# Kernel optimization log

Measured on AMD Instinct MI355X. Metric: run time of the kernel, lower is better.

Reference implementation:

```python
import jax, jax.numpy as jnp
import numpy as np
from jax import lax

B, T = 64, 2048
D_LSTM, D_ENC, D_ATT, N_F, K = 1024, 512, 128, 32, 31
PAD = (K - 1) // 2  # 15, 'same' padding as Tacotron2 LocationLayer


def setup_inputs() -> dict:
    key = jax.random.key(0)
    ks = jax.random.split(key, 11)
    def w(k, shape, fan_in):
        return jax.random.normal(k, shape, dtype=jnp.float32) / np.sqrt(fan_in)
    return {
        "query": jax.random.normal(ks[0], (B, 1, D_LSTM), dtype=jnp.float32),
        "memory": jax.random.normal(ks[1], (B, T, D_ENC), dtype=jnp.float32),
        "attention_weights_cat": jax.random.uniform(ks[2], (B, 2, T), dtype=jnp.float32),
        "Wq": w(ks[3], (D_ATT, D_LSTM), D_LSTM),
        "bq": jnp.zeros((D_ATT,), jnp.float32),
        "Wm": w(ks[4], (D_ATT, D_ENC), D_ENC),
        "bm": jnp.zeros((D_ATT,), jnp.float32),
        "Wconv": w(ks[5], (N_F, 2, K), 2 * K),  # Conv1d weight [out, in, k], bias=False
        "Wloc": w(ks[6], (D_ATT, N_F), N_F),     # location dense, bias=False
        "Wv": w(ks[7], (1, D_ATT), D_ATT),
        "bv": jnp.zeros((1,), jnp.float32),
    }


def reference(query, memory, attention_weights_cat, Wq, bq, Wm, bm, Wconv, Wloc, Wv, bv):
    # query_layer: [B,1,D_LSTM] -> [B,1,D_ATT]
    q = query @ Wq.T + bq
    # memory_layer: [B,T,D_ENC] -> [B,T,D_ATT]
    k = memory @ Wm.T + bm
    # location_layer: Conv1d same-pad over time, then dense to D_ATT
    conv = lax.conv_general_dilated(
        attention_weights_cat, Wconv, window_strides=(1,),
        padding=[(PAD, PAD)], dimension_numbers=("NCH", "OIH", "NCH"))  # [B,N_F,T]
    loc = jnp.einsum("bft,af->bta", conv, Wloc)  # [B,T,D_ATT]
    # energies: v^T tanh(q + k + loc) -> [B,T]
    energies = (jnp.tanh(q + k + loc) @ Wv.T + bv).squeeze(-1)
    attention_weights = jax.nn.softmax(energies, axis=1)  # [B,T]
    attention_context = jnp.einsum("bt,btd->bd", attention_weights, memory)  # [B,D_ENC]
    return attention_context, attention_weights
```

## Files before the change

kernel.cpp:

```cpp
#include <hip/hip_runtime.h>
#include <math.h>

#define B_ 64
#define T_ 2048
#define DL 1024
#define DE 512
#define DA 128
#define NF 32
#define KW 31
#define PADW 15
#define TT 128

typedef short bf16x8 __attribute__((ext_vector_type(8)));
typedef float f32x4 __attribute__((ext_vector_type(4)));

__device__ __forceinline__ void split_bf16(float x, unsigned short &hi, unsigned short &lo) {
    unsigned u = __float_as_uint(x);
    unsigned short h = (unsigned short)((u + 0x7FFFu + ((u >> 16) & 1u)) >> 16);
    float hf = __uint_as_float((unsigned)h << 16);
    float l = x - hf;
    unsigned ul = __float_as_uint(l);
    hi = h;
    lo = (unsigned short)((ul + 0x7FFFu + ((ul >> 16) & 1u)) >> 16);
}

__device__ __forceinline__ void split8(const float4 &v0, const float4 &v1, bf16x8 &hi, bf16x8 &lo) {
    unsigned short h, l;
    split_bf16(v0.x, h, l); hi[0] = (short)h; lo[0] = (short)l;
    split_bf16(v0.y, h, l); hi[1] = (short)h; lo[1] = (short)l;
    split_bf16(v0.z, h, l); hi[2] = (short)h; lo[2] = (short)l;
    split_bf16(v0.w, h, l); hi[3] = (short)h; lo[3] = (short)l;
    split_bf16(v1.x, h, l); hi[4] = (short)h; lo[4] = (short)l;
    split_bf16(v1.y, h, l); hi[5] = (short)h; lo[5] = (short)l;
    split_bf16(v1.z, h, l); hi[6] = (short)h; lo[6] = (short)l;
    split_bf16(v1.w, h, l); hi[7] = (short)h; lo[7] = (short)l;
}

__device__ __forceinline__ float fast_tanh(float x) {
    x = fminf(fmaxf(x, -15.f), 15.f);
    float e2 = __expf(2.f * x);
    return (e2 - 1.f) * __builtin_amdgcn_rcpf(e2 + 1.f);
}

__device__ __forceinline__ void gload_lds16(const float* g, float* l) {
    __builtin_amdgcn_global_load_lds((const __attribute__((address_space(1))) void*)g,
                                     (__attribute__((address_space(3))) void*)l, 16, 0, 0);
}

__global__ __launch_bounds__(256) void prep_kernel(const float* __restrict__ Wm,
                                                   const float* __restrict__ Wloc,
                                                   unsigned short* __restrict__ bg_hi,
                                                   unsigned short* __restrict__ bg_lo,
                                                   unsigned short* __restrict__ bw_hi,
                                                   unsigned short* __restrict__ bw_lo) {
    int i = blockIdx.x * 256 + threadIdx.x;
    unsigned short h, l;
    if (i < DA * DE) {
        split_bf16(Wm[i], h, l);
        bg_hi[i] = h;
        bg_lo[i] = l;
    } else {
        int j = i - DA * DE;
        split_bf16(Wloc[j], h, l);
        bw_hi[j] = h;
        bw_lo[j] = l;
    }
}

__global__ __launch_bounds__(128) void q_kernel(const float* __restrict__ query,
                                                const float* __restrict__ Wq,
                                                const float* __restrict__ bq,
                                                float* __restrict__ qbuf) {
    int b = blockIdx.x;
    int a = threadIdx.x;
    __shared__ __align__(16) float qs[DL];
    for (int i = threadIdx.x; i < DL; i += 128) qs[i] = query[(size_t)b * DL + i];
    __syncthreads();
    const float* wrow = Wq + (size_t)a * DL;
    float acc = 0.f;
#pragma unroll 8
    for (int i = 0; i < DL; i += 4) {
        float4 w = *(const float4*)(wrow + i);
        float4 q4 = *(const float4*)(qs + i);
        acc += w.x * q4.x + w.y * q4.y + w.z * q4.z + w.w * q4.w;
    }
    qbuf[(size_t)b * DA + a] = acc + bq[a];
}

__global__ __launch_bounds__(256, 3) void energy_kernel(
    const float* __restrict__ mem,
    const float* __restrict__ attw,
    const unsigned short* __restrict__ bg_hi,
    const unsigned short* __restrict__ bg_lo,
    const unsigned short* __restrict__ bw_hi,
    const unsigned short* __restrict__ bw_lo,
    const float* __restrict__ bm,
    const float* __restrict__ Wconv,
    const float* __restrict__ Wv,
    const float* __restrict__ bv,
    const float* __restrict__ qbuf,
    float* __restrict__ e_out)
{
    __shared__ __align__(16) float Ast[2][TT * NF];
    __shared__ __align__(16) float attw_s[2 * 160];
    __shared__ __align__(16) float wconv_s[NF * 64];
    __shared__ float qb_s[DA], wv_s[DA];
    __shared__ float e_part[2][TT];

    const int tid = threadIdx.x;
    const int b = blockIdx.y;
    const int t0 = blockIdx.x * TT;
    const int lane = tid & 63;
    const int wave = tid >> 6;
    const int wm = wave & 1, wn = wave >> 1;
    const int m = lane & 15;
    const int g = lane >> 4;
    const int q8 = g * 8;
    const int s0 = g * 2;

    if (tid < DA) {
        qb_s[tid] = qbuf[(size_t)b * DA + tid] + bm[tid];
        wv_s[tid] = Wv[tid];
    }

    for (int i = tid; i < 2 * (TT + KW - 1); i += 256) {
        int c = i / 158, j = i % 158;
        int t = t0 - PADW + j;
        attw_s[c * 160 + j] = (t >= 0 && t < T_) ? attw[((size_t)b * 2 + c) * T_ + t] : 0.f;
    }
    for (int i = tid; i < NF * 2 * KW; i += 256) {
        int f = i / 62, r = i % 62;
        wconv_s[f * 64 + r] = Wconv[i];
    }
    __syncthreads();

    for (int i = tid; i < TT * NF; i += 256) {
        int t = i >> 5, f = i & 31;
        const float* w0 = wconv_s + f * 64;
        const float* a0 = attw_s + t;
        const float* a1 = attw_s + 160 + t;
        float s = 0.f;
#pragma unroll
        for (int k = 0; k < KW; ++k) s += w0[k] * a0[k] + w0[31 + k] * a1[k];
        Ast[0][t * 32 + (((f >> 2) ^ (t & 7)) << 2) + (f & 3)] = s;
    }

    const size_t mem_base = ((size_t)b * T_ + t0) * DE;

#pragma unroll
    for (int r = 0; r < 4; ++r) {
        int idx = tid + 256 * r;
        int t = idx >> 3, sp = idx & 7;
        gload_lds16(mem + mem_base + (size_t)t * DE + ((sp ^ (t & 7)) << 2),
                    &Ast[1][idx << 2]);
    }

    bf16x8 bh[4], bl[4];
#pragma unroll
    for (int ni = 0; ni < 4; ++ni) {
        int a = wn * 64 + ni * 16 + m;
        bh[ni] = *(const bf16x8*)(bw_hi + a * NF + q8);
        bl[ni] = *(const bf16x8*)(bw_lo + a * NF + q8);
    }

    asm volatile("s_waitcnt lgkmcnt(0)\n\ts_barrier" ::: "memory");

    f32x4 acc[4][4];
#pragma unroll
    for (int mi = 0; mi < 4; ++mi)
#pragma unroll
        for (int ni = 0; ni < 4; ++ni) {
            f32x4 z = {0.f, 0.f, 0.f, 0.f};
            acc[mi][ni] = z;
        }

    auto compute = [&](const float* buf) {
        bf16x8 ah[4], al[4];
#pragma unroll
        for (int mi = 0; mi < 4; ++mi) {
            int t = wm * 64 + mi * 16 + m;
            int tx = t & 7;
            const float* rowp = buf + t * 32;
            float4 v0 = *(const float4*)(rowp + ((s0 ^ tx) << 2));
            float4 v1 = *(const float4*)(rowp + (((s0 + 1) ^ tx) << 2));
            split8(v0, v1, ah[mi], al[mi]);
        }
        __builtin_amdgcn_s_setprio(1);
#pragma unroll
        for (int ni = 0; ni < 4; ++ni)
#pragma unroll
            for (int mi = 0; mi < 4; ++mi) {
                acc[mi][ni] = __builtin_amdgcn_mfma_f32_16x16x32_bf16(ah[mi], bh[ni], acc[mi][ni], 0, 0, 0);
                acc[mi][ni] = __builtin_amdgcn_mfma_f32_16x16x32_bf16(ah[mi], bl[ni], acc[mi][ni], 0, 0, 0);
                acc[mi][ni] = __builtin_amdgcn_mfma_f32_16x16x32_bf16(al[mi], bh[ni], acc[mi][ni], 0, 0, 0);
            }
        __builtin_amdgcn_s_setprio(0);
    };

    compute(&Ast[0][0]);

#pragma unroll 1
    for (int c = 0; c < 16; ++c) {
        const int k0 = c * 32;
#pragma unroll
        for (int ni = 0; ni < 4; ++ni) {
            int a = wn * 64 + ni * 16 + m;
            bh[ni] = *(const bf16x8*)(bg_hi + (size_t)a * DE + k0 + q8);
            bl[ni] = *(const bf16x8*)(bg_lo + (size_t)a * DE + k0 + q8);
        }
        asm volatile("s_waitcnt vmcnt(4)\n\ts_barrier" ::: "memory");
        {
            const int k0n = ((c + 1) & 15) * 32;
            const float* gk = mem + mem_base + k0n;
            float* lb = &Ast[c & 1][0];
#pragma unroll
            for (int r = 0; r < 4; ++r) {
                int idx = tid + 256 * r;
                int t = idx >> 3, sp = idx & 7;
                gload_lds16(gk + (size_t)t * DE + ((sp ^ (t & 7)) << 2), lb + (idx << 2));
            }
        }
        compute(&Ast[(c + 1) & 1][0]);
    }

    __syncthreads();
    float wvr[4], qbr[4];
#pragma unroll
    for (int ni = 0; ni < 4; ++ni) {
        int a = wn * 64 + ni * 16 + m;
        wvr[ni] = wv_s[a];
        qbr[ni] = qb_s[a];
    }
    float bvv = bv[0];
#pragma unroll
    for (int mi = 0; mi < 4; ++mi) {
#pragma unroll
        for (int reg = 0; reg < 4; ++reg) {
            float s = 0.f;
#pragma unroll
            for (int ni = 0; ni < 4; ++ni)
                s += wvr[ni] * fast_tanh(acc[mi][ni][reg] + qbr[ni]);
            s += __shfl_xor(s, 1, 64);
            s += __shfl_xor(s, 2, 64);
            s += __shfl_xor(s, 4, 64);
            s += __shfl_xor(s, 8, 64);
            if (m == 0)
                e_part[wn][wm * 64 + mi * 16 + (lane >> 4) * 4 + reg] = s;
        }
    }
    __syncthreads();
    if (tid < TT)
        e_out[(size_t)b * T_ + t0 + tid] = e_part[0][tid] + e_part[1][tid] + bvv;
}

__global__ __launch_bounds__(256) void softmax_kernel(const float* __restrict__ e,
                                                      float* __restrict__ wout) {
    int b = blockIdx.x;
    int tid = threadIdx.x;
    __shared__ float red[4];
    float v[8];
    float m = -1e30f;
#pragma unroll
    for (int r = 0; r < 8; ++r) {
        v[r] = e[(size_t)b * T_ + r * 256 + tid];
        m = fmaxf(m, v[r]);
    }
#pragma unroll
    for (int off = 1; off < 64; off <<= 1) m = fmaxf(m, __shfl_xor(m, off, 64));
    if ((tid & 63) == 0) red[tid >> 6] = m;
    __syncthreads();
    m = fmaxf(fmaxf(red[0], red[1]), fmaxf(red[2], red[3]));
    __syncthreads();
    float s = 0.f;
#pragma unroll
    for (int r = 0; r < 8; ++r) {
        v[r] = expf(v[r] - m);
        s += v[r];
    }
#pragma unroll
    for (int off = 1; off < 64; off <<= 1) s += __shfl_xor(s, off, 64);
    if ((tid & 63) == 0) red[tid >> 6] = s;
    __syncthreads();
    s = red[0] + red[1] + red[2] + red[3];
    float inv = 1.0f / s;
#pragma unroll
    for (int r = 0; r < 8; ++r) wout[(size_t)b * T_ + r * 256 + tid] = v[r] * inv;
}

__global__ __launch_bounds__(256) void ctx_partial_kernel(const float* __restrict__ mem,
                                                          const float* __restrict__ w,
                                                          float* __restrict__ partial) {
    int b = blockIdx.y, tc = blockIdx.x;
    int tid = threadIdx.x;
    __shared__ float ws_s[128];
    __shared__ float red[512];
    if (tid < 128) ws_s[tid] = w[(size_t)b * T_ + tc * 128 + tid];
    __syncthreads();
    int d = (tid & 127) * 4;
    int th = tid >> 7;
    const float* mp = mem + ((size_t)b * T_ + tc * 128 + th * 64) * DE + d;
    float a0 = 0.f, a1 = 0.f, a2 = 0.f, a3 = 0.f;
#pragma unroll 8
    for (int t = 0; t < 64; ++t) {
        float4 v = *(const float4*)(mp + (size_t)t * DE);
        float wv = ws_s[th * 64 + t];
        a0 += wv * v.x; a1 += wv * v.y; a2 += wv * v.z; a3 += wv * v.w;
    }
    if (th == 1) {
        float* r = red + (tid & 127) * 4;
        r[0] = a0; r[1] = a1; r[2] = a2; r[3] = a3;
    }
    __syncthreads();
    if (th == 0) {
        const float* r = red + tid * 4;
        float* pp = partial + ((size_t)b * 16 + tc) * DE + d;
        pp[0] = a0 + r[0]; pp[1] = a1 + r[1]; pp[2] = a2 + r[2]; pp[3] = a3 + r[3];
    }
}

__global__ __launch_bounds__(512) void ctx_reduce_kernel(const float* __restrict__ partial,
                                                         float* __restrict__ ctx) {
    int b = blockIdx.x;
    int d = threadIdx.x;
    float s = 0.f;
#pragma unroll
    for (int j = 0; j < 16; ++j) s += partial[((size_t)b * 16 + j) * DE + d];
    ctx[(size_t)b * DE + d] = s;
}

extern "C" void kernel_launch(void* const* d_in, const int* in_sizes, int n_in,
                              void* d_out, int out_size, void* d_ws, size_t ws_size,
                              hipStream_t stream) {
    const float* query  = (const float*)d_in[0];
    const float* memory = (const float*)d_in[1];
    const float* attw   = (const float*)d_in[2];
    const float* Wq     = (const float*)d_in[3];
    const float* bq     = (const float*)d_in[4];
    const float* Wm     = (const float*)d_in[5];
    const float* bm     = (const float*)d_in[6];
    const float* Wconv  = (const float*)d_in[7];
    const float* Wloc   = (const float*)d_in[8];
    const float* Wv     = (const float*)d_in[9];
    const float* bv     = (const float*)d_in[10];

    float* out = (float*)d_out;
    float* ctx_out = out;
    float* w_out = out + B_ * DE;

    float* ws = (float*)d_ws;
    float* qbuf = ws;
    float* ebuf = qbuf + B_ * DA;
    float* partial = ebuf + (size_t)B_ * T_;
    unsigned short* bg_hi = (unsigned short*)(partial + (size_t)B_ * 16 * DE);
    unsigned short* bg_lo = bg_hi + DA * DE;
    unsigned short* bw_hi = bg_lo + DA * DE;
    unsigned short* bw_lo = bw_hi + DA * NF;

    prep_kernel<<<dim3((DA * DE + DA * NF) / 256), dim3(256), 0, stream>>>(
        Wm, Wloc, bg_hi, bg_lo, bw_hi, bw_lo);
    q_kernel<<<dim3(B_), dim3(128), 0, stream>>>(query, Wq, bq, qbuf);
    energy_kernel<<<dim3(T_ / TT, B_), dim3(256), 0, stream>>>(
        memory, attw, bg_hi, bg_lo, bw_hi, bw_lo, bm, Wconv, Wv, bv, qbuf, ebuf);
    softmax_kernel<<<dim3(B_), dim3(256), 0, stream>>>(ebuf, w_out);
    ctx_partial_kernel<<<dim3(16, B_), dim3(256), 0, stream>>>(memory, w_out, partial);
    ctx_reduce_kernel<<<dim3(B_), dim3(512), 0, stream>>>(partial, ctx_out);
}
```

Measured before the change: 574.4 us.

## Load memory tiles directly into registers, dropping LDS staging and barriers

The main GEMM loop stops staging memory tiles in LDS through async global-to-LDS copies. Each wave now loads its A fragments (fp32 memory rows) and B fragments (bf16 hi/lo weights) straight from global memory into registers, using a two-deep register double buffer and no per-chunk barriers. The conv result is pre-split into bf16 hi/lo in a padded LDS layout, and launch bounds drop to 2 blocks per SM to make room for the larger register set. The cost is uncoalesced strided global loads (16-byte reads per row), duplicate loads of A across the two wn waves, and lower occupancy.

Measured after the change: 548.7 us. 4.5% less time.

```diff
diff --git a/kernel.cpp b/kernel.cpp
--- a/kernel.cpp
+++ b/kernel.cpp
@@ -10,6 +10,7 @@
 #define KW 31
 #define PADW 15
 #define TT 128
+#define LDA 40
 
 typedef short bf16x8 __attribute__((ext_vector_type(8)));
 typedef float f32x4 __attribute__((ext_vector_type(4)));
@@ -40,11 +41,6 @@
     x = fminf(fmaxf(x, -15.f), 15.f);
     float e2 = __expf(2.f * x);
     return (e2 - 1.f) * __builtin_amdgcn_rcpf(e2 + 1.f);
-}
-
-__device__ __forceinline__ void gload_lds16(const float* g, float* l) {
-    __builtin_amdgcn_global_load_lds((const __attribute__((address_space(1))) void*)g,
-                                     (__attribute__((address_space(3))) void*)l, 16, 0, 0);
 }
 
 __global__ __launch_bounds__(256) void prep_kernel(const float* __restrict__ Wm,
@@ -87,7 +83,7 @@
     qbuf[(size_t)b * DA + a] = acc + bq[a];
 }
 
-__global__ __launch_bounds__(256, 3) void energy_kernel(
+__global__ __launch_bounds__(256, 2) void energy_kernel(
     const float* __restrict__ mem,
     const float* __restrict__ attw,
     const unsigned short* __restrict__ bg_hi,
@@ -101,7 +97,8 @@
     const float* __restrict__ qbuf,
     float* __restrict__ e_out)
 {
-    __shared__ __align__(16) float Ast[2][TT * NF];
+    __shared__ __align__(16) unsigned short Ahi[TT * LDA];
+    __shared__ __align__(16) unsigned short Alo[TT * LDA];
     __shared__ __align__(16) float attw_s[2 * 160];
     __shared__ __align__(16) float wconv_s[NF * 64];
     __shared__ float qb_s[DA], wv_s[DA];
@@ -116,7 +113,6 @@
     const int m = lane & 15;
     const int g = lane >> 4;
     const int q8 = g * 8;
-    const int s0 = g * 2;
 
     if (tid < DA) {
         qb_s[tid] = qbuf[(size_t)b * DA + tid] + bm[tid];
@@ -142,28 +138,42 @@
         float s = 0.f;
 #pragma unroll
         for (int k = 0; k < KW; ++k) s += w0[k] * a0[k] + w0[31 + k] * a1[k];
-        Ast[0][t * 32 + (((f >> 2) ^ (t & 7)) << 2) + (f & 3)] = s;
-    }
-
-    const size_t mem_base = ((size_t)b * T_ + t0) * DE;
-
-#pragma unroll
-    for (int r = 0; r < 4; ++r) {
-        int idx = tid + 256 * r;
-        int t = idx >> 3, sp = idx & 7;
-        gload_lds16(mem + mem_base + (size_t)t * DE + ((sp ^ (t & 7)) << 2),
-                    &Ast[1][idx << 2]);
-    }
-
-    bf16x8 bh[4], bl[4];
+        unsigned short h, l;
+        split_bf16(s, h, l);
+        Ahi[t * LDA + f] = h;
+        Alo[t * LDA + f] = l;
+    }
+
+    bf16x8 cbh[4], cbl[4];
 #pragma unroll
     for (int ni = 0; ni < 4; ++ni) {
         int a = wn * 64 + ni * 16 + m;
-        bh[ni] = *(const bf16x8*)(bw_hi + a * NF + q8);
-        bl[ni] = *(const bf16x8*)(bw_lo + a * NF + q8);
-    }
-
-    asm volatile("s_waitcnt lgkmcnt(0)\n\ts_barrier" ::: "memory");
+        cbh[ni] = *(const bf16x8*)(bw_hi + a * NF + q8);
+        cbl[ni] = *(const bf16x8*)(bw_lo + a * NF + q8);
+    }
+    __syncthreads();
+
+    const size_t mem_base = ((size_t)b * T_ + t0) * DE;
+    const float* ap = mem + mem_base + (size_t)(wm * 64 + m) * DE + q8;
+    const unsigned short* bhp = bg_hi + (size_t)(wn * 64 + m) * DE + q8;
+    const unsigned short* blp = bg_lo + (size_t)(wn * 64 + m) * DE + q8;
+
+    float4 aA[4][2];
+    float4 aB[4][2];
+    bf16x8 bhA[4], blA[4], bhB[4], blB[4];
+#pragma unroll
+    for (int mi = 0; mi < 4; ++mi) {
+        const float* p = ap + (size_t)mi * 16 * DE;
+        aA[mi][0] = *(const float4*)(p);
+        aA[mi][1] = *(const float4*)(p + 4);
+    }
+#pragma unroll
+    for (int ni = 0; ni < 4; ++ni) {
+        const unsigned short* ph = bhp + (size_t)ni * 16 * DE;
+        const unsigned short* pl = blp + (size_t)ni * 16 * DE;
+        bhA[ni] = *(const bf16x8*)(ph);
+        blA[ni] = *(const bf16x8*)(pl);
+    }
 
     f32x4 acc[4][4];
 #pragma unroll
@@ -174,56 +184,91 @@
             acc[mi][ni] = z;
         }
 
-    auto compute = [&](const float* buf) {
+    {
         bf16x8 ah[4], al[4];
 #pragma unroll
         for (int mi = 0; mi < 4; ++mi) {
-            int t = wm * 64 + mi * 16 + m;
-            int tx = t & 7;
-            const float* rowp = buf + t * 32;
-            float4 v0 = *(const float4*)(rowp + ((s0 ^ tx) << 2));
-            float4 v1 = *(const float4*)(rowp + (((s0 + 1) ^ tx) << 2));
-            split8(v0, v1, ah[mi], al[mi]);
+            int r = (wm * 64 + mi * 16 + m) * LDA + q8;
+            ah[mi] = *(const bf16x8*)(Ahi + r);
+            al[mi] = *(const bf16x8*)(Alo + r);
         }
         __builtin_amdgcn_s_setprio(1);
 #pragma unroll
         for (int ni = 0; ni < 4; ++ni)
 #pragma unroll
             for (int mi = 0; mi < 4; ++mi) {
-                acc[mi][ni] = __builtin_amdgcn_mfma_f32_16x16x32_bf16(ah[mi], bh[ni], acc[mi][ni], 0, 0, 0);
-                acc[mi][ni] = __builtin_amdgcn_mfma_f32_16x16x32_bf16(ah[mi], bl[ni], acc[mi][ni], 0, 0, 0);
-                acc[mi][ni] = __builtin_amdgcn_mfma_f32_16x16x32_bf16(al[mi], bh[ni], acc[mi][ni], 0, 0, 0);
+                acc[mi][ni] = __builtin_amdgcn_mfma_f32_16x16x32_bf16(ah[mi], cbh[ni], acc[mi][ni], 0, 0, 0);
+                acc[mi][ni] = __builtin_amdgcn_mfma_f32_16x16x32_bf16(ah[mi], cbl[ni], acc[mi][ni], 0, 0, 0);
+                acc[mi][ni] = __builtin_amdgcn_mfma_f32_16x16x32_bf16(al[mi], cbh[ni], acc[mi][ni], 0, 0, 0);
             }
         __builtin_amdgcn_s_setprio(0);
-    };
-
-    compute(&Ast[0][0]);
+    }
 
 #pragma unroll 1
-    for (int c = 0; c < 16; ++c) {
-        const int k0 = c * 32;
-#pragma unroll
-        for (int ni = 0; ni < 4; ++ni) {
-            int a = wn * 64 + ni * 16 + m;
-            bh[ni] = *(const bf16x8*)(bg_hi + (size_t)a * DE + k0 + q8);
-            bl[ni] = *(const bf16x8*)(bg_lo + (size_t)a * DE + k0 + q8);
+    for (int it = 0; it < 8; ++it) {
+        const int c = it * 2;
+        {
+            bf16x8 ah[4], al[4];
+#pragma unroll
+            for (int mi = 0; mi < 4; ++mi) split8(aA[mi][0], aA[mi][1], ah[mi], al[mi]);
+            const float* apn = ap + (c + 1) * 32;
+            const unsigned short* bhn = bhp + (c + 1) * 32;
+            const unsigned short* bln = blp + (c + 1) * 32;
+#pragma unroll
+            for (int mi = 0; mi < 4; ++mi) {
+                const float* p = apn + (size_t)mi * 16 * DE;
+                aB[mi][0] = *(const float4*)(p);
+                aB[mi][1] = *(const float4*)(p + 4);
+            }
+#pragma unroll
+            for (int ni = 0; ni < 4; ++ni) {
+                bhB[ni] = *(const bf16x8*)(bhn + (size_t)ni * 16 * DE);
+                blB[ni] = *(const bf16x8*)(bln + (size_t)ni * 16 * DE);
+            }
+            __builtin_amdgcn_s_setprio(1);
+#pragma unroll
+            for (int ni = 0; ni < 4; ++ni)
+#pragma unroll
+                for (int mi = 0; mi < 4; ++mi) {
+                    acc[mi][ni] = __builtin_amdgcn_mfma_f32_16x16x32_bf16(ah[mi], bhA[ni], acc[mi][ni], 0, 0, 0);
+                    acc[mi][ni] = __builtin_amdgcn_mfma_f32_16x16x32_bf16(ah[mi], blA[ni], acc[mi][ni], 0, 0, 0);
+                    acc[mi][ni] = __builtin_amdgcn_mfma_f32_16x16x32_bf16(al[mi], bhA[ni], acc[mi][ni], 0, 0, 0);
+                }
+            __builtin_amdgcn_s_setprio(0);
         }
-        asm volatile("s_waitcnt vmcnt(4)\n\ts_barrier" ::: "memory");
         {
-            const int k0n = ((c + 1) & 15) * 32;
-            const float* gk = mem + mem_base + k0n;
-            float* lb = &Ast[c & 1][0];
-#pragma unroll
-            for (int r = 0; r < 4; ++r) {
-                int idx = tid + 256 * r;
-                int t = idx >> 3, sp = idx & 7;
-                gload_lds16(gk + (size_t)t * DE + ((sp ^ (t & 7)) << 2), lb + (idx << 2));
+            bf16x8 ah[4], al[4];
+#pragma unroll
+            for (int mi = 0; mi < 4; ++mi) split8(aB[mi][0], aB[mi][1], ah[mi], al[mi]);
+            if (it < 7) {
+                const float* apn = ap + (c + 2) * 32;
+                const unsigned short* bhn = bhp + (c + 2) * 32;
+                const unsigned short* bln = blp + (c + 2) * 32;
+#pragma unroll
+                for (int mi = 0; mi < 4; ++mi) {
+                    const float* p = apn + (size_t)mi * 16 * DE;
+                    aA[mi][0] = *(const float4*)(p);
+                    aA[mi][1] = *(const float4*)(p + 4);
+                }
+#pragma unroll
+                for (int ni = 0; ni < 4; ++ni) {
+                    bhA[ni] = *(const bf16x8*)(bhn + (size_t)ni * 16 * DE);
+                    blA[ni] = *(const bf16x8*)(bln + (size_t)ni * 16 * DE);
+                }
             }
+            __builtin_amdgcn_s_setprio(1);
+#pragma unroll
+            for (int ni = 0; ni < 4; ++ni)
+#pragma unroll
+                for (int mi = 0; mi < 4; ++mi) {
+                    acc[mi][ni] = __builtin_amdgcn_mfma_f32_16x16x32_bf16(ah[mi], bhB[ni], acc[mi][ni], 0, 0, 0);
+                    acc[mi][ni] = __builtin_amdgcn_mfma_f32_16x16x32_bf16(ah[mi], blB[ni], acc[mi][ni], 0, 0, 0);
+                    acc[mi][ni] = __builtin_amdgcn_mfma_f32_16x16x32_bf16(al[mi], bhB[ni], acc[mi][ni], 0, 0, 0);
+                }
+            __builtin_amdgcn_s_setprio(0);
         }
-        compute(&Ast[(c + 1) & 1][0]);
-    }
-
-    __syncthreads();
+    }
+
     float wvr[4], qbr[4];
 #pragma unroll
     for (int ni = 0; ni < 4; ++ni) {
```
